# Performance work log

Hardware: AMD Instinct MI355X
Metric: run time of the kernel (lower is better)

## Reference

```python
import jax, jax.numpy as jnp
import numpy as np

N, D, E = 50000, 128, 100000
H1, H2, H3 = 8, 8, 4
NEG_SLOPE = 0.2  # PyG GATv2Conv default negative_slope


def _gatv2_layer(x, src, dst, Wl, Wr, att, b, heads):
    # GATv2Conv(in=D, out=D, heads=heads, concat=False), share_weights=False
    C = Wl.shape[1] // heads
    xl = (x @ Wl).reshape(-1, heads, C)  # source-side transform (x_j)
    xr = (x @ Wr).reshape(-1, heads, C)  # target-side transform (x_i)
    m = jax.nn.leaky_relu(xl[src] + xr[dst], NEG_SLOPE)      # [E,H,C]
    e = jnp.einsum('ehc,hc->eh', m, att)                      # [E,H]
    # segment softmax over incoming edges of each destination node
    emax = jax.ops.segment_max(e, dst, num_segments=N)        # [N,H]
    a = jnp.exp(e - emax[dst])
    denom = jax.ops.segment_sum(a, dst, num_segments=N)       # [N,H] (>0: self-loops)
    a = a / denom[dst]
    out = jax.ops.segment_sum(xl[src] * a[:, :, None], dst, num_segments=N)  # [N,H,C]
    return out.mean(axis=1) + b  # concat=False -> head mean, then bias


def setup_inputs() -> dict:
    key = jax.random.key(0)
    ks = jax.random.split(key, 16)
    x = jax.random.normal(ks[0], (N, D), dtype=jnp.float32)
    src = jax.random.randint(ks[1], (E,), 0, N)
    dst = jax.random.randint(ks[2], (E,), 0, N)
    src = jnp.where(src == dst, (src + 1) % N, src)  # no pre-existing self loops
    edge_index = jnp.stack([src, dst]).astype(jnp.int64)
    s = 1.0 / np.sqrt(D)
    def lin(k, h):
        return jax.random.uniform(k, (D, h * D), jnp.float32, -s, s)
    def attn(k, h):
        return jax.random.uniform(k, (h, D), jnp.float32, -s, s)
    return {
        'x': x, 'edge_index': edge_index,
        'W1l': lin(ks[3], H1), 'W1r': lin(ks[4], H1), 'att1': attn(ks[5], H1), 'b1': jnp.zeros((D,), jnp.float32),
        'W2l': lin(ks[6], H2), 'W2r': lin(ks[7], H2), 'att2': attn(ks[8], H2), 'b2': jnp.zeros((D,), jnp.float32),
        'W3l': lin(ks[9], H3), 'W3r': lin(ks[10], H3), 'att3': attn(ks[11], H3), 'b3': jnp.zeros((D,), jnp.float32),
    }


def reference(x, edge_index, W1l, W1r, att1, b1, W2l, W2r, att2, b2, W3l, W3r, att3, b3):
    # PyG GATv2Conv adds self loops by default
    loops = jnp.arange(N, dtype=edge_index.dtype)
    src = jnp.concatenate([edge_index[0], loops])
    dst = jnp.concatenate([edge_index[1], loops])
    h = x + _gatv2_layer(x, src, dst, W1l, W1r, att1, b1, H1)
    h = jax.nn.elu(h)  # dropout is identity in eval mode
    h = h + _gatv2_layer(h, src, dst, W2l, W2r, att2, b2, H2)
    h = jax.nn.elu(h)
    h = h + _gatv2_layer(h, src, dst, W3l, W3r, att3, b3, H3)
    return h
```

## Files before the change

### kernel.cpp

```cpp
#include <hip/hip_runtime.h>

#define NN 50000
#define DD 128
#define EE 100000
#define ET (EE + NN)

typedef __attribute__((ext_vector_type(4))) float f32x4;
typedef __attribute__((ext_vector_type(8))) short bf16x8;
typedef __attribute__((ext_vector_type(4))) unsigned short u16x4;
typedef __attribute__((ext_vector_type(4))) unsigned int u32x4;

static __device__ __forceinline__ unsigned short f2bf(float f) {
  union { float f; unsigned int u; } v; v.f = f;
  unsigned int r = (v.u + 0x7FFFu + ((v.u >> 16) & 1u)) >> 16;
  return (unsigned short)r;
}
static __device__ __forceinline__ float bflo(unsigned int u) {
  union { unsigned int u; float f; } v; v.u = u << 16; return v.f;
}
static __device__ __forceinline__ float bfhi(unsigned int u) {
  union { unsigned int u; float f; } v; v.u = u & 0xffff0000u; return v.f;
}

__global__ __launch_bounds__(256) void k_prep(
    const float* __restrict__ x,
    const float* __restrict__ W1l, const float* __restrict__ W1r,
    const float* __restrict__ W2l, const float* __restrict__ W2r,
    const float* __restrict__ W3l, const float* __restrict__ W3r,
    const float* __restrict__ att1, const float* __restrict__ att2, const float* __restrict__ att3,
    unsigned short* __restrict__ wt1, unsigned short* __restrict__ wt2,
    unsigned short* __restrict__ wt3,
    float* __restrict__ as1, float* __restrict__ as2, float* __restrict__ as3,
    unsigned short* __restrict__ abf, int* __restrict__ counts) {
  const int i = blockIdx.x * 256 + threadIdx.x;
  const float LOG2E = 1.4426950408889634f;
  if (i < 262144) {
    int half = i >> 17, rem = i & 131071;
    int nn = rem >> 7, k = rem & 127;
    const float* W = half ? W1r : W1l;
    wt1[i] = f2bf(W[(size_t)k * 1024 + nn]);
  } else if (i < 524288) {
    int local = i - 262144;
    int half = local >> 17, rem = local & 131071;
    int nn = rem >> 7, k = rem & 127;
    const float* W = half ? W2r : W2l;
    wt2[local] = f2bf(W[(size_t)k * 1024 + nn]);
  } else if (i < 655360) {
    int local = i - 524288;
    int half = local >> 16, rem = local & 65535;
    int nn = rem >> 7, k = rem & 127;
    const float* W = half ? W3r : W3l;
    wt3[local] = f2bf(W[(size_t)k * 512 + nn]);
  } else if (i < 657920) {
    int local = i - 655360;
    if (local < 1024) as1[local] = att1[local] * LOG2E;
    else if (local < 2048) as2[local - 1024] = att2[local - 1024] * LOG2E;
    else as3[local - 2048] = att3[local - 2048] * LOG2E;
  } else if (i < 707920) {
    counts[i - 657920] = 0;
  } else if (i < 2307920) {
    int u = i - 707920;
    f32x4 v = *(const f32x4*)(x + (size_t)u * 4);
    u16x4 w;
    w.x = f2bf(v.x); w.y = f2bf(v.y); w.z = f2bf(v.z); w.w = f2bf(v.w);
    *(u16x4*)(abf + (size_t)u * 4) = w;
  }
}

__global__ void k_count(const int* __restrict__ ei, int* __restrict__ counts) {
  int i = blockIdx.x * blockDim.x + threadIdx.x;
  if (i >= ET) return;
  int dst = (i < EE) ? ei[EE + i] : (i - EE);
  if (dst < 0 || dst >= NN) return;
  atomicAdd(&counts[dst], 1);
}

__global__ __launch_bounds__(1024) void k_scan(const int* __restrict__ counts,
                                               int* __restrict__ offs,
                                               int* __restrict__ cursor) {
  __shared__ int wsum[16];
  __shared__ int wpre[16];
  __shared__ int wtot;
  const int tid = threadIdx.x;
  const int wv = tid >> 6, lane = tid & 63;
  int carry = 0;
  for (int base = 0; base < NN; base += 4096) {
    int i0 = base + tid * 4;
    int v[4];
#pragma unroll
    for (int q = 0; q < 4; ++q) { int i = i0 + q; v[q] = (i < NN) ? counts[i] : 0; }
    int s = v[0] + v[1] + v[2] + v[3];
    int sc = s;
#pragma unroll
    for (int m = 1; m < 64; m <<= 1) {
      int t = __shfl_up(sc, m, 64);
      if (lane >= m) sc += t;
    }
    if (lane == 63) wsum[wv] = sc;
    __syncthreads();
    if (tid < 16) {
      int t = wsum[tid];
      int scc = t;
#pragma unroll
      for (int m = 1; m < 16; m <<= 1) {
        int u = __shfl_up(scc, m, 64);
        if (tid >= m) scc += u;
      }
      wpre[tid] = scc - t;
      if (tid == 15) wtot = scc;
    }
    __syncthreads();
    int excl = carry + wpre[wv] + (sc - s);
#pragma unroll
    for (int q = 0; q < 4; ++q) {
      int i = i0 + q;
      if (i < NN) { offs[i] = excl; cursor[i] = excl; }
      excl += v[q];
    }
    carry += wtot;
    __syncthreads();
  }
  if (tid == 0) offs[NN] = carry;
}

__global__ void k_fill(const int* __restrict__ ei, int* __restrict__ cursor,
                       int* __restrict__ srcs) {
  int i = blockIdx.x * blockDim.x + threadIdx.x;
  if (i >= ET) return;
  int src, dst;
  if (i < EE) { src = ei[i]; dst = ei[EE + i]; }
  else { src = dst = i - EE; }
  if (dst < 0 || dst >= NN) return;
  if (src < 0 || src >= NN) src = dst;
  int pos = atomicAdd(&cursor[dst], 1);
  if (pos >= 0 && pos < ET) srcs[pos] = src;
}

__global__ __launch_bounds__(256) void gemm_bt(
    const unsigned short* __restrict__ A, const unsigned short* __restrict__ WT,
    unsigned short* __restrict__ Cl, unsigned short* __restrict__ Cr,
    int M, int Nout, int lgny) {
  const int f = blockIdx.x;
  const int c = f & ((1 << lgny) - 1);
  const int x = f >> lgny;
  const int z = c & 1, y = c >> 1;
  const int m0 = x * 128, n0 = y * 128;
  unsigned short* C = z ? Cr : Cl;
  const unsigned short* BT = WT + (size_t)z * Nout * DD;

  __shared__ unsigned short As[128 * 128];
  __shared__ unsigned short Bs[128 * 128];
  const int tid = threadIdx.x;
  const int wave = tid >> 6, lane = tid & 63;
  const int hi = lane >> 4, lr = lane & 15;

#pragma unroll
  for (int i = 0; i < 8; ++i) {
    int row = i * 16 + wave * 4 + hi;
    int c16 = lr ^ (row & 7);
    const unsigned short* ga = A + (size_t)(m0 + row) * DD + c16 * 8;
    __builtin_amdgcn_global_load_lds((const __attribute__((address_space(1))) void*)ga,
        (__attribute__((address_space(3))) void*)(As + i * 2048 + wave * 512), 16, 0, 0);
    const unsigned short* gb = BT + (size_t)(n0 + row) * DD + c16 * 8;
    __builtin_amdgcn_global_load_lds((const __attribute__((address_space(1))) void*)gb,
        (__attribute__((address_space(3))) void*)(Bs + i * 2048 + wave * 512), 16, 0, 0);
  }
  __syncthreads();

  const int wr = (wave >> 1) * 64, wc = (wave & 1) * 64;
  f32x4 acc[4][4];
#pragma unroll
  for (int i = 0; i < 4; ++i)
#pragma unroll
    for (int j = 0; j < 4; ++j) acc[i][j] = (f32x4){0.f, 0.f, 0.f, 0.f};

#pragma unroll
  for (int k0 = 0; k0 < 128; k0 += 32) {
    const int ck = (k0 >> 3) + hi;
    bf16x8 af[4], bfr[4];
#pragma unroll
    for (int mi = 0; mi < 4; ++mi) {
      int r = wr + mi * 16 + lr;
      af[mi] = *(const bf16x8*)&As[r * 128 + ((ck ^ (r & 7)) << 3)];
    }
#pragma unroll
    for (int ni = 0; ni < 4; ++ni) {
      int cc = wc + ni * 16 + lr;
      bfr[ni] = *(const bf16x8*)&Bs[cc * 128 + ((ck ^ (cc & 7)) << 3)];
    }
#pragma unroll
    for (int mi = 0; mi < 4; ++mi)
#pragma unroll
      for (int ni = 0; ni < 4; ++ni)
        acc[mi][ni] = __builtin_amdgcn_mfma_f32_16x16x32_bf16(af[mi], bfr[ni], acc[mi][ni], 0, 0, 0);
  }

#pragma unroll
  for (int mi = 0; mi < 4; ++mi) {
#pragma unroll
    for (int ni = 0; ni < 4; ++ni) {
      int col = n0 + wc + ni * 16 + lr;
#pragma unroll
      for (int j = 0; j < 4; ++j) {
        int row = m0 + wr + mi * 16 + (hi << 2) + j;
        if (row < M) C[(size_t)row * Nout + col] = f2bf(acc[mi][ni][j]);
      }
    }
  }
}

template <int H>
__global__ __launch_bounds__(256) void gat_agg3(
    const unsigned short* __restrict__ xl, const unsigned short* __restrict__ xr,
    const int* __restrict__ offs, const int* __restrict__ srcs,
    const float* __restrict__ att_s,
    const float* __restrict__ bias,
    const float* __restrict__ resid, float* __restrict__ out,
    unsigned short* __restrict__ hbf, int do_elu) {
  constexpr int LPH = 64 / H;
  constexpr int CPL = 2 * H;
  constexpr int NW = H;
  constexpr int ROW = H * DD;
  const int wave = threadIdx.x >> 6, lane = threadIdx.x & 63;
  const int n = blockIdx.x * 4 + wave;
  if (n >= NN) return;
  const int cb = lane * CPL;

  float xrv[CPL], av[CPL];
  {
    const unsigned int* q = (const unsigned int*)(xr + (size_t)n * ROW + cb);
#pragma unroll
    for (int w = 0; w < NW; ++w) {
      unsigned int u = q[w];
      xrv[2 * w] = bflo(u);
      xrv[2 * w + 1] = bfhi(u);
    }
#pragma unroll
    for (int c = 0; c < CPL; ++c) av[c] = att_s[cb + c];
  }

  float acc[CPL];
#pragma unroll
  for (int c = 0; c < CPL; ++c) acc[c] = 0.f;
  float mx = -1e30f, dn = 0.f;

  const int e0 = offs[n], e1 = offs[n + 1];
  for (int j = e0; j < e1; j += 4) {
    const int B = (e1 - j < 4) ? (e1 - j) : 4;
    unsigned int rows[4][NW];
#pragma unroll
    for (int b = 0; b < 4; ++b) {
      if (b < B) {
        int s = srcs[j + b];
        const unsigned int* qq = (const unsigned int*)(xl + (size_t)s * ROW + cb);
#pragma unroll
        for (int w = 0; w < NW; ++w) rows[b][w] = qq[w];
      }
    }
    float p[4];
#pragma unroll
    for (int b = 0; b < 4; ++b) {
      float pp = -1e30f;
      if (b < B) {
        pp = 0.f;
#pragma unroll
        for (int w = 0; w < NW; ++w) {
          float x0 = bflo(rows[b][w]), x1 = bfhi(rows[b][w]);
          float z0 = x0 + xrv[2 * w]; z0 = fmaxf(z0, 0.2f * z0);
          float z1 = x1 + xrv[2 * w + 1]; z1 = fmaxf(z1, 0.2f * z1);
          pp = fmaf(z0, av[2 * w], pp);
          pp = fmaf(z1, av[2 * w + 1], pp);
        }
#pragma unroll
        for (int m = 1; m < LPH; m <<= 1) pp += __shfl_xor(pp, m, 64);
      }
      p[b] = pp;
    }
    float pm = fmaxf(fmaxf(p[0], p[1]), fmaxf(p[2], p[3]));
    if (__any(pm > mx + 11.5f)) {
      float mnew = fmaxf(mx, pm);
      float sc = __builtin_amdgcn_exp2f(mx - mnew);
      dn *= sc;
#pragma unroll
      for (int c = 0; c < CPL; ++c) acc[c] *= sc;
      mx = mnew;
    }
#pragma unroll
    for (int b = 0; b < 4; ++b) {
      if (b < B) {
        float wt = __builtin_amdgcn_exp2f(p[b] - mx);
        dn += wt;
#pragma unroll
        for (int w = 0; w < NW; ++w) {
          acc[2 * w] = fmaf(wt, bflo(rows[b][w]), acc[2 * w]);
          acc[2 * w + 1] = fmaf(wt, bfhi(rows[b][w]), acc[2 * w + 1]);
        }
      }
    }
  }

  float r[CPL];
  const float inv = (1.f / (float)H) / dn;
#pragma unroll
  for (int c = 0; c < CPL; ++c) r[c] = acc[c] * inv;
#pragma unroll
  for (int m = LPH; m < 64; m <<= 1)
#pragma unroll
    for (int c = 0; c < CPL; ++c) r[c] += __shfl_xor(r[c], m, 64);

  if (lane < LPH) {
    float o[CPL];
#pragma unroll
    for (int c = 0; c < CPL; ++c) {
      o[c] = r[c] + bias[cb + c] + resid[(size_t)n * DD + cb + c];
      if (do_elu && o[c] < 0.f)
        o[c] = __builtin_amdgcn_exp2f(o[c] * 1.4426950408889634f) - 1.f;
    }
#pragma unroll
    for (int c = 0; c < CPL; c += 4) {
      f32x4 v; v.x = o[c]; v.y = o[c + 1]; v.z = o[c + 2]; v.w = o[c + 3];
      *(f32x4*)(out + (size_t)n * DD + cb + c) = v;
    }
    if (hbf) {
#pragma unroll
      for (int c = 0; c < CPL; c += 8) {
        u32x4 pk;
#pragma unroll
        for (int q = 0; q < 4; ++q)
          pk[q] = (unsigned int)f2bf(o[c + 2 * q]) | ((unsigned int)f2bf(o[c + 2 * q + 1]) << 16);
        *(u32x4*)(hbf + (size_t)n * DD + cb + c) = pk;
      }
    }
  }
}

extern "C" void kernel_launch(void* const* d_in, const int* in_sizes, int n_in,
                              void* d_out, int out_size, void* d_ws, size_t ws_size,
                              hipStream_t stream) {
  const float* x = (const float*)d_in[0];
  const int* ei = (const int*)d_in[1];
  const float* W1l = (const float*)d_in[2];
  const float* W1r = (const float*)d_in[3];
  const float* att1 = (const float*)d_in[4];
  const float* b1 = (const float*)d_in[5];
  const float* W2l = (const float*)d_in[6];
  const float* W2r = (const float*)d_in[7];
  const float* att2 = (const float*)d_in[8];
  const float* b2 = (const float*)d_in[9];
  const float* W3l = (const float*)d_in[10];
  const float* W3r = (const float*)d_in[11];
  const float* att3 = (const float*)d_in[12];
  const float* b3 = (const float*)d_in[13];
  float* out = (float*)d_out;

  char* p = (char*)d_ws;
  auto carve = [&](size_t bytes) {
    char* r = p;
    p += (bytes + 255) & ~(size_t)255;
    return r;
  };
  unsigned short* xl = (unsigned short*)carve((size_t)NN * 1024 * 2);
  unsigned short* xr = (unsigned short*)carve((size_t)NN * 1024 * 2);
  unsigned short* abf = (unsigned short*)carve((size_t)NN * DD * 2);
  unsigned short* wt1 = (unsigned short*)carve((size_t)2 * 1024 * DD * 2);
  unsigned short* wt2 = (unsigned short*)carve((size_t)2 * 1024 * DD * 2);
  unsigned short* wt3 = (unsigned short*)carve((size_t)2 * 512 * DD * 2);
  float* as1 = (float*)carve((size_t)8 * DD * 4);
  float* as2 = (float*)carve((size_t)8 * DD * 4);
  float* as3 = (float*)carve((size_t)4 * DD * 4);
  int* counts = (int*)carve((size_t)NN * 4);
  int* offs = (int*)carve(((size_t)NN + 1) * 4);
  int* cursor = (int*)carve((size_t)NN * 4);
  int* srcs = (int*)carve((size_t)ET * 4);
  size_t needed = (size_t)(p - (char*)d_ws);
  if (needed > ws_size) return;

  k_prep<<<9016, 256, 0, stream>>>(x, W1l, W1r, W2l, W2r, W3l, W3r, att1, att2, att3,
                                   wt1, wt2, wt3, as1, as2, as3, abf, counts);
  k_count<<<(ET + 255) / 256, 256, 0, stream>>>(ei, counts);
  k_scan<<<1, 1024, 0, stream>>>(counts, offs, cursor);
  k_fill<<<(ET + 255) / 256, 256, 0, stream>>>(ei, cursor, srcs);

  const int gx = (NN + 127) / 128;
  gemm_bt<<<gx * 16, 256, 0, stream>>>(abf, wt1, xl, xr, NN, 1024, 4);
  gat_agg3<8><<<(NN + 3) / 4, 256, 0, stream>>>(xl, xr, offs, srcs, as1, b1, x, out, abf, 1);
  gemm_bt<<<gx * 16, 256, 0, stream>>>(abf, wt2, xl, xr, NN, 1024, 4);
  gat_agg3<8><<<(NN + 3) / 4, 256, 0, stream>>>(xl, xr, offs, srcs, as2, b2, out, out, abf, 1);
  gemm_bt<<<gx * 8, 256, 0, stream>>>(abf, wt3, xl, xr, NN, 512, 3);
  gat_agg3<4><<<(NN + 3) / 4, 256, 0, stream>>>(xl, xr, offs, srcs, as3, b3, out, out, nullptr, 0);
}
```

Baseline: 492.1 us.

## Split each node's heads across two waves and combine halves via LDS

The GATv2 aggregation kernel now gives each destination node two waves, each handling half the heads (half of the row width), instead of one wave covering all heads. The partial head-mean results from the second wave are written to shared memory and, after a block barrier, added by the first wave, which then applies bias, residual and ELU and writes the fp32 and bf16 outputs. The aim is to halve per-lane registers and double the waves available to hide gather latency. In exchange, every edge's source index and softmax bookkeeping is processed by two waves, and a block-wide barrier plus an LDS exchange are added.

```diff
diff --git a/kernel.cpp b/kernel.cpp
--- a/kernel.cpp
+++ b/kernel.cpp
@@ -9,6 +9,7 @@
 typedef __attribute__((ext_vector_type(8))) short bf16x8;
 typedef __attribute__((ext_vector_type(4))) unsigned short u16x4;
 typedef __attribute__((ext_vector_type(4))) unsigned int u32x4;
+typedef __attribute__((ext_vector_type(2))) unsigned int u32x2;
 
 static __device__ __forceinline__ unsigned short f2bf(float f) {
   union { float f; unsigned int u; } v; v.f = f;
@@ -210,21 +211,24 @@
 }
 
 template <int H>
-__global__ __launch_bounds__(256) void gat_agg3(
+__global__ __launch_bounds__(256) void gat_agg4(
     const unsigned short* __restrict__ xl, const unsigned short* __restrict__ xr,
     const int* __restrict__ offs, const int* __restrict__ srcs,
     const float* __restrict__ att_s,
     const float* __restrict__ bias,
     const float* __restrict__ resid, float* __restrict__ out,
     unsigned short* __restrict__ hbf, int do_elu) {
-  constexpr int LPH = 64 / H;
-  constexpr int CPL = 2 * H;
-  constexpr int NW = H;
+  constexpr int HG = H / 2;
+  constexpr int CPL = 2 * HG;
+  constexpr int NW = HG;
+  constexpr int LPH = 128 / CPL;
   constexpr int ROW = H * DD;
+  constexpr int HALFROW = ROW / 2;
   const int wave = threadIdx.x >> 6, lane = threadIdx.x & 63;
-  const int n = blockIdx.x * 4 + wave;
+  const int nsub = wave >> 1, g = wave & 1;
+  const int n = blockIdx.x * 2 + nsub;
   if (n >= NN) return;
-  const int cb = lane * CPL;
+  const int cb = g * HALFROW + lane * CPL;
 
   float xrv[CPL], av[CPL];
   {
@@ -308,27 +312,37 @@
 #pragma unroll
     for (int c = 0; c < CPL; ++c) r[c] += __shfl_xor(r[c], m, 64);
 
-  if (lane < LPH) {
+  __shared__ float lds[2][DD];
+  const int d0 = (lane * CPL) & 127;
+  if (g == 1 && lane < LPH) {
+#pragma unroll
+    for (int c = 0; c < CPL; ++c) lds[nsub][d0 + c] = r[c];
+  }
+  __syncthreads();
+  if (g == 0 && lane < LPH) {
     float o[CPL];
 #pragma unroll
     for (int c = 0; c < CPL; ++c) {
-      o[c] = r[c] + bias[cb + c] + resid[(size_t)n * DD + cb + c];
+      o[c] = r[c] + lds[nsub][d0 + c] + bias[d0 + c] + resid[(size_t)n * DD + d0 + c];
       if (do_elu && o[c] < 0.f)
         o[c] = __builtin_amdgcn_exp2f(o[c] * 1.4426950408889634f) - 1.f;
     }
 #pragma unroll
     for (int c = 0; c < CPL; c += 4) {
       f32x4 v; v.x = o[c]; v.y = o[c + 1]; v.z = o[c + 2]; v.w = o[c + 3];
-      *(f32x4*)(out + (size_t)n * DD + cb + c) = v;
+      *(f32x4*)(out + (size_t)n * DD + d0 + c) = v;
     }
     if (hbf) {
-#pragma unroll
-      for (int c = 0; c < CPL; c += 8) {
-        u32x4 pk;
-#pragma unroll
-        for (int q = 0; q < 4; ++q)
-          pk[q] = (unsigned int)f2bf(o[c + 2 * q]) | ((unsigned int)f2bf(o[c + 2 * q + 1]) << 16);
-        *(u32x4*)(hbf + (size_t)n * DD + cb + c) = pk;
+      unsigned int pk[CPL / 2];
+#pragma unroll
+      for (int q = 0; q < CPL / 2; ++q)
+        pk[q] = (unsigned int)f2bf(o[2 * q]) | ((unsigned int)f2bf(o[2 * q + 1]) << 16);
+      if constexpr (CPL == 8) {
+        u32x4 v; v.x = pk[0]; v.y = pk[1]; v.z = pk[2]; v.w = pk[3];
+        *(u32x4*)(hbf + (size_t)n * DD + d0) = v;
+      } else {
+        u32x2 v; v.x = pk[0]; v.y = pk[1];
+        *(u32x2*)(hbf + (size_t)n * DD + d0) = v;
       }
     }
   }
@@ -382,10 +396,11 @@
   k_fill<<<(ET + 255) / 256, 256, 0, stream>>>(ei, cursor, srcs);
 
   const int gx = (NN + 127) / 128;
+  const int ga = (NN + 1) / 2;
   gemm_bt<<<gx * 16, 256, 0, stream>>>(abf, wt1, xl, xr, NN, 1024, 4);
-  gat_agg3<8><<<(NN + 3) / 4, 256, 0, stream>>>(xl, xr, offs, srcs, as1, b1, x, out, abf, 1);
+  gat_agg4<8><<<ga, 256, 0, stream>>>(xl, xr, offs, srcs, as1, b1, x, out, abf, 1);
   gemm_bt<<<gx * 16, 256, 0, stream>>>(abf, wt2, xl, xr, NN, 1024, 4);
-  gat_agg3<8><<<(NN + 3) / 4, 256, 0, stream>>>(xl, xr, offs, srcs, as2, b2, out, out, abf, 1);
+  gat_agg4<8><<<ga, 256, 0, stream>>>(xl, xr, offs, srcs, as2, b2, out, out, abf, 1);
   gemm_bt<<<gx * 8, 256, 0, stream>>>(abf, wt3, xl, xr, NN, 512, 3);
-  gat_agg3<4><<<(NN + 3) / 4, 256, 0, stream>>>(xl, xr, offs, srcs, as3, b3, out, out, nullptr, 0);
-}
+  gat_agg4<4><<<ga, 256, 0, stream>>>(xl, xr, offs, srcs, as3, b3, out, out, nullptr, 0);
+}
```

Result: no change. 495.1 us (+0.6%).
